# Optimization experiments

Hardware: AMD Instinct MI355X
Metric: run time of the kernel (lower is better)

Reference implementation:

```python
import jax, jax.numpy as jnp
import numpy as np

N, K, D = 262144, 1024, 64


def setup_inputs() -> dict:
    key = jax.random.key(0)
    k1, k2 = jax.random.split(key)
    input_data = jax.random.normal(k1, (N, D), dtype=jnp.float32)
    codewords = jax.random.normal(k2, (K, D), dtype=jnp.float32)
    return {"input_data": input_data, "codewords": codewords}


def reference(input_data, codewords):
    # input_data: [N, D], codewords: [K, D]
    x = input_data.reshape(-1, codewords.shape[1])
    x2 = jnp.sum(x * x, axis=1, keepdims=True)          # [N, 1]
    c2 = jnp.sum(codewords * codewords, axis=1)          # [K]
    d2 = x2 + c2[None, :] - 2.0 * (x @ codewords.T)      # [N, K]
    distances = jnp.sqrt(jnp.maximum(d2, 0.0))
    quantized_indices = jnp.argmin(distances, axis=1)    # [N] int
    quantized_distances = jnp.take_along_axis(
        distances, quantized_indices[:, None], axis=1
    )[:, 0]                                              # [N]
    quantized_data = codewords[quantized_indices]        # [N, D]
    return (quantized_indices, quantized_distances, quantized_data)
```

## Files before the change

### kernel.cpp

```cpp
#include <hip/hip_runtime.h>


#define N_PTS 262144
#define K_CW  1024
#define DIM   64
#define CHUNK_B 36864

typedef __attribute__((ext_vector_type(8)))  short short8;
typedef __attribute__((ext_vector_type(16))) float floatx16;

__device__ __forceinline__ unsigned short f2bf(float f) {
    unsigned u = __float_as_uint(f);
    return (unsigned short)((u + 0x7FFFu + ((u >> 16) & 1u)) >> 16);
}
__device__ __forceinline__ float bf2f(unsigned short h) {
    return __uint_as_float(((unsigned)h) << 16);
}
__device__ __forceinline__ float dot4(float4 a, float4 b) {
    return a.x*b.x + a.y*b.y + a.z*b.z + a.w*b.w;
}
__device__ __forceinline__ void async_cp16(const void* g, void* l) {
    __builtin_amdgcn_global_load_lds(
        (const __attribute__((address_space(1))) unsigned int*)g,
        (__attribute__((address_space(3))) unsigned int*)l, 16, 0, 0);
}

__global__ void vq_prep(const float* __restrict__ cw, unsigned char* __restrict__ ws) {
    const int k = blockIdx.x * 256 + threadIdx.x;
    const int ch = k >> 7, r = k & 127;
    unsigned short* chunk = (unsigned short*)(ws + (size_t)ch * CHUNK_B);
    unsigned short* hi = chunk + r * 72;
    unsigned short* lo = hi + 9216;
    const float4* cr = (const float4*)cw + (size_t)k * 16;
    float c2 = 0.f;
    #pragma unroll
    for (int j = 0; j < 16; ++j) {
        float4 v = cr[j];
        c2 += dot4(v, v);
        float4 m = make_float4(-2.f*v.x, -2.f*v.y, -2.f*v.z, -2.f*v.w);
        unsigned short h0 = f2bf(m.x), h1 = f2bf(m.y), h2 = f2bf(m.z), h3 = f2bf(m.w);
        unsigned short l0 = f2bf(m.x - bf2f(h0)), l1 = f2bf(m.y - bf2f(h1)),
                       l2 = f2bf(m.z - bf2f(h2)), l3 = f2bf(m.w - bf2f(h3));
        uint2 hv, lv;
        hv.x = (unsigned)h0 | ((unsigned)h1 << 16);
        hv.y = (unsigned)h2 | ((unsigned)h3 << 16);
        lv.x = (unsigned)l0 | ((unsigned)l1 << 16);
        lv.y = (unsigned)l2 | ((unsigned)l3 << 16);
        *(uint2*)(hi + j * 4) = hv;
        *(uint2*)(lo + j * 4) = lv;
    }
    *(float*)(hi + 64) = c2;
}

__launch_bounds__(256, 2)
__global__ void vq_kernel(const float* __restrict__ x,
                          const float* __restrict__ cw,
                          const unsigned char* __restrict__ ws,
                          float* __restrict__ out) {
    __shared__ __align__(16) unsigned char sB[2 * CHUNK_B];
    int*   sci  = (int*)sB;
    float* sdd  = (float*)(sB + 2048);
    int*   sidx = (int*)(sB + 4096);

    const int tid  = threadIdx.x;
    const int w    = tid >> 6;
    const int lane = tid & 63;
    const int q    = lane >> 5;
    const int l31  = lane & 31;
    const int base = blockIdx.x * 256;
    const float4* __restrict__ x4  = (const float4*)x;
    const float4* __restrict__ c4p = (const float4*)cw;

    const int start = ((blockIdx.x ^ (blockIdx.x >> 8)) & 3) * 2;

    {
        const unsigned char* g = ws + (size_t)start * CHUNK_B + w * 9216 + lane * 16;
        unsigned char* l = sB + w * 9216;
        #pragma unroll
        for (int i = 0; i < 9; ++i) async_cp16(g + i * 1024, l + i * 1024);
    }

    short8 ah[2][4], al[2][4];
    #pragma unroll
    for (int rt = 0; rt < 2; ++rt) {
        const int row = w * 64 + rt * 32 + l31;
        const float4* xr = x4 + (size_t)(base + row) * 16;
        #pragma unroll
        for (int ks = 0; ks < 4; ++ks) {
            float4 va = xr[ks * 4 + q * 2];
            float4 vb = xr[ks * 4 + q * 2 + 1];
            float f[8] = {va.x, va.y, va.z, va.w, vb.x, vb.y, vb.z, vb.w};
            short8 h, l;
            #pragma unroll
            for (int j = 0; j < 8; ++j) {
                unsigned short hb = f2bf(f[j]);
                h[j] = (short)hb;
                l[j] = (short)f2bf(f[j] - bf2f(hb));
            }
            ah[rt][ks] = h; al[rt][ks] = l;
        }
    }

    float bu[32];
    #pragma unroll
    for (int s = 0; s < 32; ++s) bu[s] = 3.4e38f;

    for (int i = 0; i < 8; ++i) {
        const int ch = (start + i) & 7;
        __syncthreads();

        if (i < 7) {
            const int nx = (start + i + 1) & 7;
            const unsigned char* g = ws + (size_t)nx * CHUNK_B + w * 9216 + lane * 16;
            unsigned char* l = sB + ((i + 1) & 1) * CHUNK_B + w * 9216;
            #pragma unroll
            for (int j = 0; j < 9; ++j) async_cp16(g + j * 1024, l + j * 1024);
        }

        const unsigned short* bufS = (const unsigned short*)(sB + (i & 1) * CHUNK_B);

        #pragma unroll
        for (int ct = 0; ct < 4; ++ct) {
            const int nrow = ct * 32 + l31;
            short8 bh[4], bl[4];
            #pragma unroll
            for (int ks = 0; ks < 4; ++ks) {
                bh[ks] = *(const short8*)&bufS[nrow * 72 + ks * 16 + q * 8];
                bl[ks] = *(const short8*)&bufS[9216 + nrow * 72 + ks * 16 + q * 8];
            }
            const float c2v = *(const float*)&bufS[nrow * 72 + 64];
            floatx16 a0, a1;
            #pragma unroll
            for (int r = 0; r < 16; ++r) { a0[r] = c2v; a1[r] = c2v; }
            __builtin_amdgcn_s_setprio(1);
            #pragma unroll
            for (int ks = 0; ks < 4; ++ks) {
                a0 = __builtin_amdgcn_mfma_f32_32x32x16_bf16(ah[0][ks], bh[ks], a0, 0, 0, 0);
                a1 = __builtin_amdgcn_mfma_f32_32x32x16_bf16(ah[1][ks], bh[ks], a1, 0, 0, 0);
                a0 = __builtin_amdgcn_mfma_f32_32x32x16_bf16(al[0][ks], bh[ks], a0, 0, 0, 0);
                a1 = __builtin_amdgcn_mfma_f32_32x32x16_bf16(al[1][ks], bh[ks], a1, 0, 0, 0);
                a0 = __builtin_amdgcn_mfma_f32_32x32x16_bf16(ah[0][ks], bl[ks], a0, 0, 0, 0);
                a1 = __builtin_amdgcn_mfma_f32_32x32x16_bf16(ah[1][ks], bl[ks], a1, 0, 0, 0);
            }
            __builtin_amdgcn_s_setprio(0);
            const unsigned tch = (unsigned)(ch * 4 + ct);
            #pragma unroll
            for (int r = 0; r < 16; ++r) {
                unsigned u0 = (__float_as_uint(a0[r]) & 0xFFFFFFE0u) | tch;
                bu[r] = fminf(bu[r], __uint_as_float(u0));
                unsigned u1 = (__float_as_uint(a1[r]) & 0xFFFFFFE0u) | tch;
                bu[16 + r] = fminf(bu[16 + r], __uint_as_float(u1));
            }
        }
    }
    __syncthreads();

    #pragma unroll
    for (int s = 0; s < 32; ++s) {
        float b0 = bu[s];
        int i0 = (int)(((__float_as_uint(b0) & 31u) << 5) | (unsigned)l31);
        float b1 = 3.4e38f; int i1 = 0x7fffffff;
        #pragma unroll
        for (int m = 1; m < 32; m <<= 1) {
            float ob0 = __shfl_xor(b0, m); int oi0 = __shfl_xor(i0, m);
            float ob1 = __shfl_xor(b1, m); int oi1 = __shfl_xor(i1, m);
            bool t = (ob0 < b0) || (ob0 == b0 && oi0 < i0);
            float hs = t ? b0 : ob0; int hi_ = t ? i0 : oi0;
            b0 = t ? ob0 : b0;       i0 = t ? oi0 : i0;
            bool u = (ob1 < b1) || (ob1 == b1 && oi1 < i1);
            float ms = u ? ob1 : b1; int mi = u ? oi1 : i1;
            bool z = (hs < ms) || (hs == ms && hi_ < mi);
            b1 = z ? hs : ms; i1 = z ? hi_ : mi;
        }
        if (l31 == s) {
            const int rt = s >> 4, r = s & 15;
            const int row = w * 64 + rt * 32 + (r & 3) + 8 * (r >> 2) + 4 * q;
            sci[row * 2]     = i0;
            sci[row * 2 + 1] = i1;
        }
    }
    __syncthreads();

    #pragma unroll
    for (int it = 0; it < 2; ++it) {
        const int pid = it * 128 + (tid >> 1);
        const int h   = tid & 1;
        const int ia = sci[pid * 2], ib = sci[pid * 2 + 1];
        const float4* xr = x4 + (size_t)(base + pid) * 16 + h * 8;
        const float4* ca = c4p + (size_t)ia * 16 + h * 8;
        const float4* cb = c4p + (size_t)ib * 16 + h * 8;
        float da = 0.f, db = 0.f;
        #pragma unroll
        for (int j = 0; j < 8; ++j) {
            float4 xv = xr[j], av = ca[j], bv = cb[j];
            float4 d1 = make_float4(xv.x-av.x, xv.y-av.y, xv.z-av.z, xv.w-av.w);
            float4 d2 = make_float4(xv.x-bv.x, xv.y-bv.y, xv.z-bv.z, xv.w-bv.w);
            da += dot4(d1, d1);
            db += dot4(d2, d2);
        }
        da += __shfl_xor(da, 1);
        db += __shfl_xor(db, 1);
        if (h == 0) { sdd[pid * 2] = da; sdd[pid * 2 + 1] = db; }
    }
    __syncthreads();

    {
        const float da = sdd[tid * 2], db = sdd[tid * 2 + 1];
        const int   ia = sci[tid * 2], ib = sci[tid * 2 + 1];
        bool ta = (da < db) || (da == db && ia < ib);
        const int   bidx = ta ? ia : ib;
        const float bd   = ta ? da : db;
        out[base + tid]         = (float)bidx;
        out[N_PTS + base + tid] = sqrtf(fmaxf(bd, 0.f));
        sidx[tid] = bidx;
    }
    __syncthreads();

    {
        float4* od = (float4*)(out + 2 * (size_t)N_PTS) + (size_t)base * 16;
        #pragma unroll
        for (int i = 0; i < 16; ++i) {
            const int g = i * 256 + tid;
            od[g] = c4p[(size_t)sidx[g >> 4] * 16 + (g & 15)];
        }
    }
}

extern "C" void kernel_launch(void* const* d_in, const int* in_sizes, int n_in,
                              void* d_out, int out_size, void* d_ws, size_t ws_size,
                              hipStream_t stream) {
    const float* x  = (const float*)d_in[0];
    const float* cw = (const float*)d_in[1];
    float* out = (float*)d_out;
    unsigned char* ws = (unsigned char*)d_ws;
    vq_prep<<<4, 256, 0, stream>>>(cw, ws);
    vq_kernel<<<N_PTS / 256, 256, 0, stream>>>(x, cw, ws, out);
}
```

Before: 254.4 us.

## Split codebook into resident LDS halves across blocks, merge with extra kernels

The main kernel now has 1024-thread blocks. Each block loads half of the preprocessed codebook (144 KB) into LDS once and keeps it there, which removes the per-chunk double-buffered streaming. Each block handles 2048 points against that half. The top-2 selection now uses min-shuffles plus ballots, and partial results (index and squared distance per half) are written to scratch space in the output buffer. Two small follow-up kernels merge the halves and gather the codewords, adding launches and extra global traffic; because there is one 1024-thread block per CU, occupancy is low, and the merge's tie-break on index order may differ from the original.

New measurement: 662.4 us. 160% more time.

```diff
diff --git a/kernel.cpp b/kernel.cpp
--- a/kernel.cpp
+++ b/kernel.cpp
@@ -5,6 +5,7 @@
 #define K_CW  1024
 #define DIM   64
 #define CHUNK_B 36864
+#define HALF_B  (4 * CHUNK_B)
 
 typedef __attribute__((ext_vector_type(8)))  short short8;
 typedef __attribute__((ext_vector_type(16))) float floatx16;
@@ -52,83 +53,72 @@
     *(float*)(hi + 64) = c2;
 }
 
-__launch_bounds__(256, 2)
-__global__ void vq_kernel(const float* __restrict__ x,
-                          const float* __restrict__ cw,
-                          const unsigned char* __restrict__ ws,
-                          float* __restrict__ out) {
-    __shared__ __align__(16) unsigned char sB[2 * CHUNK_B];
-    int*   sci  = (int*)sB;
-    float* sdd  = (float*)(sB + 2048);
-    int*   sidx = (int*)(sB + 4096);
+__launch_bounds__(1024)
+__global__ void vq_main(const float* __restrict__ x,
+                        const float* __restrict__ cw,
+                        const unsigned char* __restrict__ ws,
+                        float* __restrict__ out) {
+    __shared__ __align__(16) unsigned char sB[HALF_B];
 
     const int tid  = threadIdx.x;
     const int w    = tid >> 6;
     const int lane = tid & 63;
     const int q    = lane >> 5;
     const int l31  = lane & 31;
-    const int base = blockIdx.x * 256;
+    const int half  = blockIdx.x & 1;
+    const int pbase = (blockIdx.x >> 1) * 2048;
     const float4* __restrict__ x4  = (const float4*)x;
     const float4* __restrict__ c4p = (const float4*)cw;
 
-    const int start = ((blockIdx.x ^ (blockIdx.x >> 8)) & 3) * 2;
-
     {
-        const unsigned char* g = ws + (size_t)start * CHUNK_B + w * 9216 + lane * 16;
-        unsigned char* l = sB + w * 9216;
-        #pragma unroll
-        for (int i = 0; i < 9; ++i) async_cp16(g + i * 1024, l + i * 1024);
-    }
-
-    short8 ah[2][4], al[2][4];
-    #pragma unroll
-    for (int rt = 0; rt < 2; ++rt) {
-        const int row = w * 64 + rt * 32 + l31;
-        const float4* xr = x4 + (size_t)(base + row) * 16;
-        #pragma unroll
-        for (int ks = 0; ks < 4; ++ks) {
-            float4 va = xr[ks * 4 + q * 2];
-            float4 vb = xr[ks * 4 + q * 2 + 1];
-            float f[8] = {va.x, va.y, va.z, va.w, vb.x, vb.y, vb.z, vb.w};
-            short8 h, l;
-            #pragma unroll
-            for (int j = 0; j < 8; ++j) {
-                unsigned short hb = f2bf(f[j]);
-                h[j] = (short)hb;
-                l[j] = (short)f2bf(f[j] - bf2f(hb));
-            }
-            ah[rt][ks] = h; al[rt][ks] = l;
-        }
-    }
-
-    float bu[32];
-    #pragma unroll
-    for (int s = 0; s < 32; ++s) bu[s] = 3.4e38f;
-
-    for (int i = 0; i < 8; ++i) {
-        const int ch = (start + i) & 7;
-        __syncthreads();
-
-        if (i < 7) {
-            const int nx = (start + i + 1) & 7;
-            const unsigned char* g = ws + (size_t)nx * CHUNK_B + w * 9216 + lane * 16;
-            unsigned char* l = sB + ((i + 1) & 1) * CHUNK_B + w * 9216;
-            #pragma unroll
-            for (int j = 0; j < 9; ++j) async_cp16(g + j * 1024, l + j * 1024);
-        }
-
-        const unsigned short* bufS = (const unsigned short*)(sB + (i & 1) * CHUNK_B);
-
-        #pragma unroll
-        for (int ct = 0; ct < 4; ++ct) {
-            const int nrow = ct * 32 + l31;
+        const unsigned char* g = ws + (size_t)half * HALF_B + tid * 16;
+        unsigned char* l = sB + tid * 16;
+        #pragma unroll
+        for (int s = 0; s < 9; ++s) async_cp16(g + s * 16384, l + s * 16384);
+    }
+    __syncthreads();
+
+    const unsigned short* __restrict__ S = (const unsigned short*)sB;
+
+    for (int t = 0; t < 2; ++t) {
+        const int tbase = pbase + w * 128 + t * 64;
+
+        short8 ah[2][4], al[2][4];
+        #pragma unroll
+        for (int rt = 0; rt < 2; ++rt) {
+            const int row = tbase + rt * 32 + l31;
+            const float4* xr = x4 + (size_t)row * 16;
+            #pragma unroll
+            for (int ks = 0; ks < 4; ++ks) {
+                float4 va = xr[ks * 4 + q * 2];
+                float4 vb = xr[ks * 4 + q * 2 + 1];
+                float f[8] = {va.x, va.y, va.z, va.w, vb.x, vb.y, vb.z, vb.w};
+                short8 h, l;
+                #pragma unroll
+                for (int j = 0; j < 8; ++j) {
+                    unsigned short hb = f2bf(f[j]);
+                    h[j] = (short)hb;
+                    l[j] = (short)f2bf(f[j] - bf2f(hb));
+                }
+                ah[rt][ks] = h; al[rt][ks] = l;
+            }
+        }
+
+        float bu[32];
+        #pragma unroll
+        for (int s = 0; s < 32; ++s) bu[s] = 3.4e38f;
+
+        #pragma unroll 4
+        for (int g = 0; g < 16; ++g) {
+            const unsigned short* chS = S + (g >> 2) * (CHUNK_B / 2);
+            const int nrow = (g & 3) * 32 + l31;
             short8 bh[4], bl[4];
             #pragma unroll
             for (int ks = 0; ks < 4; ++ks) {
-                bh[ks] = *(const short8*)&bufS[nrow * 72 + ks * 16 + q * 8];
-                bl[ks] = *(const short8*)&bufS[9216 + nrow * 72 + ks * 16 + q * 8];
-            }
-            const float c2v = *(const float*)&bufS[nrow * 72 + 64];
+                bh[ks] = *(const short8*)&chS[nrow * 72 + ks * 16 + q * 8];
+                bl[ks] = *(const short8*)&chS[9216 + nrow * 72 + ks * 16 + q * 8];
+            }
+            const float c2v = *(const float*)&chS[nrow * 72 + 64];
             floatx16 a0, a1;
             #pragma unroll
             for (int r = 0; r < 16; ++r) { a0[r] = c2v; a1[r] = c2v; }
@@ -143,86 +133,86 @@
                 a1 = __builtin_amdgcn_mfma_f32_32x32x16_bf16(ah[1][ks], bl[ks], a1, 0, 0, 0);
             }
             __builtin_amdgcn_s_setprio(0);
-            const unsigned tch = (unsigned)(ch * 4 + ct);
+            const unsigned tag = (unsigned)g;
             #pragma unroll
             for (int r = 0; r < 16; ++r) {
-                unsigned u0 = (__float_as_uint(a0[r]) & 0xFFFFFFE0u) | tch;
+                unsigned u0 = (__float_as_uint(a0[r]) & 0xFFFFFFE0u) | tag;
                 bu[r] = fminf(bu[r], __uint_as_float(u0));
-                unsigned u1 = (__float_as_uint(a1[r]) & 0xFFFFFFE0u) | tch;
+                unsigned u1 = (__float_as_uint(a1[r]) & 0xFFFFFFE0u) | tag;
                 bu[16 + r] = fminf(bu[16 + r], __uint_as_float(u1));
             }
         }
-    }
-    __syncthreads();
-
-    #pragma unroll
-    for (int s = 0; s < 32; ++s) {
-        float b0 = bu[s];
-        int i0 = (int)(((__float_as_uint(b0) & 31u) << 5) | (unsigned)l31);
-        float b1 = 3.4e38f; int i1 = 0x7fffffff;
-        #pragma unroll
-        for (int m = 1; m < 32; m <<= 1) {
-            float ob0 = __shfl_xor(b0, m); int oi0 = __shfl_xor(i0, m);
-            float ob1 = __shfl_xor(b1, m); int oi1 = __shfl_xor(i1, m);
-            bool t = (ob0 < b0) || (ob0 == b0 && oi0 < i0);
-            float hs = t ? b0 : ob0; int hi_ = t ? i0 : oi0;
-            b0 = t ? ob0 : b0;       i0 = t ? oi0 : i0;
-            bool u = (ob1 < b1) || (ob1 == b1 && oi1 < i1);
-            float ms = u ? ob1 : b1; int mi = u ? oi1 : i1;
-            bool z = (hs < ms) || (hs == ms && hi_ < mi);
-            b1 = z ? hs : ms; i1 = z ? hi_ : mi;
-        }
-        if (l31 == s) {
-            const int rt = s >> 4, r = s & 15;
-            const int row = w * 64 + rt * 32 + (r & 3) + 8 * (r >> 2) + 4 * q;
-            sci[row * 2]     = i0;
-            sci[row * 2 + 1] = i1;
-        }
-    }
-    __syncthreads();
-
-    #pragma unroll
-    for (int it = 0; it < 2; ++it) {
-        const int pid = it * 128 + (tid >> 1);
-        const int h   = tid & 1;
-        const int ia = sci[pid * 2], ib = sci[pid * 2 + 1];
-        const float4* xr = x4 + (size_t)(base + pid) * 16 + h * 8;
-        const float4* ca = c4p + (size_t)ia * 16 + h * 8;
-        const float4* cb = c4p + (size_t)ib * 16 + h * 8;
+
+        int keep_i0 = 0, keep_i1 = 0;
+        #pragma unroll
+        for (int s = 0; s < 32; ++s) {
+            const float v = bu[s];
+            float m1 = v;
+            #pragma unroll
+            for (int m = 1; m < 32; m <<= 1) m1 = fminf(m1, __shfl_xor(m1, m));
+            unsigned long long bm = __ballot(v == m1);
+            const int wl = __ffs((unsigned)(bm >> (q * 32))) - 1;
+            const float v2 = (l31 == wl) ? 3.4e38f : v;
+            float m2 = v2;
+            #pragma unroll
+            for (int m = 1; m < 32; m <<= 1) m2 = fminf(m2, __shfl_xor(m2, m));
+            unsigned long long bm2 = __ballot(v2 == m2);
+            const int wl2 = __ffs((unsigned)(bm2 >> (q * 32))) - 1;
+            const int i0 = (int)(((__float_as_uint(m1) & 31u) << 5) | (unsigned)wl);
+            const int i1 = (int)(((__float_as_uint(m2) & 31u) << 5) | (unsigned)wl2);
+            if (l31 == s) { keep_i0 = i0; keep_i1 = i1; }
+        }
+
+        const int rS   = l31 & 15;
+        const int prow = (l31 >> 4) * 32 + (rS & 3) + 8 * (rS >> 2) + 4 * q;
+        const int p    = tbase + prow;
+        const int ia = keep_i0, ib = keep_i1;
+        const float4* xr = x4 + (size_t)p * 16;
+        const float4* ca = c4p + (size_t)(half * 512 + ia) * 16;
+        const float4* cb = c4p + (size_t)(half * 512 + ib) * 16;
         float da = 0.f, db = 0.f;
         #pragma unroll
-        for (int j = 0; j < 8; ++j) {
+        for (int j = 0; j < 16; ++j) {
             float4 xv = xr[j], av = ca[j], bv = cb[j];
             float4 d1 = make_float4(xv.x-av.x, xv.y-av.y, xv.z-av.z, xv.w-av.w);
             float4 d2 = make_float4(xv.x-bv.x, xv.y-bv.y, xv.z-bv.z, xv.w-bv.w);
             da += dot4(d1, d1);
             db += dot4(d2, d2);
         }
-        da += __shfl_xor(da, 1);
-        db += __shfl_xor(db, 1);
-        if (h == 0) { sdd[pid * 2] = da; sdd[pid * 2 + 1] = db; }
-    }
+        const bool ta = (da < db) || (da == db && ia < ib);
+        const int   bidx = half * 512 + (ta ? ia : ib);
+        const float bd   = ta ? da : db;
+        float* Pi = out + (size_t)(2 + half * 2) * N_PTS;
+        Pi[p]         = (float)bidx;
+        Pi[N_PTS + p] = bd;
+    }
+}
+
+__launch_bounds__(256)
+__global__ void vq_merge1(float* __restrict__ out) {
+    const int p = blockIdx.x * 256 + threadIdx.x;
+    const float i0 = out[2 * (size_t)N_PTS + p];
+    const float d0 = out[3 * (size_t)N_PTS + p];
+    const float i1 = out[4 * (size_t)N_PTS + p];
+    const float d1 = out[5 * (size_t)N_PTS + p];
+    const bool ta = (d0 < d1) || (d0 == d1);
+    out[p]         = ta ? i0 : i1;
+    out[N_PTS + p] = sqrtf(fmaxf(ta ? d0 : d1, 0.f));
+}
+
+__launch_bounds__(256)
+__global__ void vq_merge2(const float* __restrict__ cw, float* __restrict__ out) {
+    __shared__ int sidx[256];
+    const int tid = threadIdx.x;
+    const int base = blockIdx.x * 256;
+    sidx[tid] = (int)out[base + tid];
     __syncthreads();
-
-    {
-        const float da = sdd[tid * 2], db = sdd[tid * 2 + 1];
-        const int   ia = sci[tid * 2], ib = sci[tid * 2 + 1];
-        bool ta = (da < db) || (da == db && ia < ib);
-        const int   bidx = ta ? ia : ib;
-        const float bd   = ta ? da : db;
-        out[base + tid]         = (float)bidx;
-        out[N_PTS + base + tid] = sqrtf(fmaxf(bd, 0.f));
-        sidx[tid] = bidx;
-    }
-    __syncthreads();
-
-    {
-        float4* od = (float4*)(out + 2 * (size_t)N_PTS) + (size_t)base * 16;
-        #pragma unroll
-        for (int i = 0; i < 16; ++i) {
-            const int g = i * 256 + tid;
-            od[g] = c4p[(size_t)sidx[g >> 4] * 16 + (g & 15)];
-        }
+    const float4* c4p = (const float4*)cw;
+    float4* od = (float4*)(out + 2 * (size_t)N_PTS) + (size_t)base * 16;
+    #pragma unroll
+    for (int i = 0; i < 16; ++i) {
+        const int g = i * 256 + tid;
+        od[g] = c4p[(size_t)sidx[g >> 4] * 16 + (g & 15)];
     }
 }
 
@@ -234,5 +224,7 @@
     float* out = (float*)d_out;
     unsigned char* ws = (unsigned char*)d_ws;
     vq_prep<<<4, 256, 0, stream>>>(cw, ws);
-    vq_kernel<<<N_PTS / 256, 256, 0, stream>>>(x, cw, ws, out);
-}
+    vq_main<<<256, 1024, 0, stream>>>(x, cw, ws, out);
+    vq_merge1<<<N_PTS / 256, 256, 0, stream>>>(out);
+    vq_merge2<<<N_PTS / 256, 256, 0, stream>>>(cw, out);
+}
```
